# Kernel tuning notes

Measured on AMD Instinct MI355X. Metric: run time of the kernel, lower is better.

Reference implementation:

```python
import jax, jax.numpy as jnp
import numpy as np

ALPHA = 0.1
K = 10


def setup_inputs() -> dict:
    key = jax.random.key(0)
    ks = jax.random.split(key, 8)
    N, E, F_IN, H, C = 100000, 1600000, 256, 128, 16
    features = jax.random.normal(ks[0], (N, F_IN), dtype=jnp.float32)
    # Kaiming-ish small init so activations stay sane
    W0 = jax.random.normal(ks[1], (F_IN, H), dtype=jnp.float32) * (1.0 / np.sqrt(F_IN))
    b0 = jnp.zeros((H,), jnp.float32)
    W1 = jax.random.normal(ks[2], (H, H), dtype=jnp.float32) * (1.0 / np.sqrt(H))
    b1 = jnp.zeros((H,), jnp.float32)
    W2 = jax.random.normal(ks[3], (H, C), dtype=jnp.float32) * (1.0 / np.sqrt(H))
    b2 = jnp.zeros((C,), jnp.float32)
    src = jax.random.randint(ks[4], (E,), 0, N, dtype=jnp.int32)
    dst = jax.random.randint(ks[5], (E,), 0, N, dtype=jnp.int32)
    return {"features": features, "W0": W0, "b0": b0, "W1": W1, "b1": b1,
            "W2": W2, "b2": b2, "src": src, "dst": dst}


def reference(features, W0, b0, W1, b1, W2, b2, src, dst):
    N = features.shape[0]
    # --- MLP feature transform (feat_drop=0 -> identity) ---
    h = jax.nn.relu(features @ W0 + b0)
    h = jax.nn.relu(h @ W1 + b1)
    h = h @ W2 + b2  # [N, C]
    # --- symmetric normalization D_out^{-1/2} A D_in^{-1/2} (DGL APPNPConv) ---
    ones = jnp.ones(src.shape[0], dtype=h.dtype)
    out_deg = jax.ops.segment_sum(ones, src, num_segments=N)
    in_deg = jax.ops.segment_sum(ones, dst, num_segments=N)
    norm_src = jnp.where(out_deg > 0, jax.lax.rsqrt(jnp.maximum(out_deg, 1.0)), 0.0)[:, None]
    norm_dst = jnp.where(in_deg > 0, jax.lax.rsqrt(jnp.maximum(in_deg, 1.0)), 0.0)[:, None]
    # --- K-step personalized PageRank propagation (edge_drop=0) ---
    h0 = h
    for _ in range(K):
        msg = (h * norm_src)[src]                         # gather [E, C]
        agg = jax.ops.segment_sum(msg, dst, num_segments=N)  # scatter-add [N, C]
        h = (1.0 - ALPHA) * (agg * norm_dst) + ALPHA * h0
    return h
```

## Files before the change

### kernel.cpp

```cpp
#include <hip/hip_runtime.h>

typedef _Float16 half8 __attribute__((ext_vector_type(8)));
typedef _Float16 half4 __attribute__((ext_vector_type(4)));
typedef float f32x4 __attribute__((ext_vector_type(4)));
typedef unsigned short u16;
typedef unsigned int u32;

constexpr int F_IN = 256;
constexpr int H    = 128;
constexpr int C    = 16;
constexpr int KITER = 10;

constexpr int RANGE = 16384;
constexpr int PCH   = 128;


__global__ __launch_bounds__(256) void hist_k(const int* __restrict__ idx,
                                              u16* __restrict__ partial,
                                              int N, int E, int R, int chunk) {
    __shared__ unsigned int cnt[RANGE / 2];
    const int p  = blockIdx.x / R;
    const int r  = blockIdx.x % R;
    const int lo = r * RANGE;
    const int hi = min(lo + RANGE, N);
    const int t  = threadIdx.x;
    for (int i = t; i < RANGE / 2; i += 256) cnt[i] = 0;
    __syncthreads();
    const int e0 = p * chunk, e1 = min(e0 + chunk, E);
    for (int e = e0 + t; e < e1; e += 256) {
        int d = idx[e];
        if (d >= lo && d < hi) {
            int dl = d - lo;
            atomicAdd(&cnt[dl >> 1], 1u << ((dl & 1) << 4));
        }
    }
    __syncthreads();
    for (int i = lo + t; i < hi; i += 256) {
        int il = i - lo;
        partial[(size_t)p * N + i] = (u16)(cnt[il >> 1] >> ((il & 1) << 4));
    }
}

__global__ __launch_bounds__(256) void colsum_k(const u16* __restrict__ partial,
                                                int* __restrict__ deg, int N) {
    int i = blockIdx.x * 256 + threadIdx.x;
    if (i < N) {
        int s = 0;
#pragma unroll 8
        for (int p = 0; p < PCH; ++p) s += partial[(size_t)p * N + i];
        deg[i] = s;
    }
}

__global__ __launch_bounds__(256) void colprefix_norm_k(u16* __restrict__ partial,
                                                        const int* __restrict__ dego,
                                                        int* __restrict__ degi,
                                                        float* __restrict__ ns,
                                                        float* __restrict__ nd, int N) {
    int i = blockIdx.x * 256 + threadIdx.x;
    if (i < N) {
        int run = 0;
        for (int p = 0; p < PCH; ++p) {
            size_t q = (size_t)p * N + i;
            int v = partial[q];
            partial[q] = (u16)run;
            run += v;
        }
        degi[i] = run;
        int a = dego[i];
        ns[i] = (a > 0) ? rsqrtf((float)a) : 0.0f;
        nd[i] = (run > 0) ? rsqrtf((float)run) : 0.0f;
    }
}


__global__ __launch_bounds__(256) void scan1(const int* __restrict__ d, int* __restrict__ off,
                                             int* __restrict__ bsum, int N) {
    __shared__ int s[256];
    int t = threadIdx.x, i = blockIdx.x * 256 + t;
    int v = (i < N) ? d[i] : 0;
    s[t] = v;
    __syncthreads();
    for (int dd = 1; dd < 256; dd <<= 1) {
        int x = (t >= dd) ? s[t - dd] : 0;
        __syncthreads();
        s[t] += x;
        __syncthreads();
    }
    if (i < N) off[i] = s[t] - v;
    if (t == 255) bsum[blockIdx.x] = s[255];
}

__global__ __launch_bounds__(512) void scan2(int* __restrict__ bsum, int nb) {
    __shared__ int s[512];
    int t = threadIdx.x;
    int v = (t < nb) ? bsum[t] : 0;
    s[t] = v;
    __syncthreads();
    for (int dd = 1; dd < 512; dd <<= 1) {
        int x = (t >= dd) ? s[t - dd] : 0;
        __syncthreads();
        s[t] += x;
        __syncthreads();
    }
    if (t < nb) bsum[t] = s[t] - v;
}

__global__ __launch_bounds__(256) void scan3(int* __restrict__ off, const int* __restrict__ bsum,
                                             int N) {
    int i = blockIdx.x * 256 + threadIdx.x;
    if (i < N) off[i] += bsum[blockIdx.x];
}


__global__ __launch_bounds__(256) void scatter2_k(const int* __restrict__ src,
                                                  const int* __restrict__ dst,
                                                  const int* __restrict__ off,
                                                  const u16* __restrict__ pprefix,
                                                  u32* __restrict__ epack,
                                                  int N, int E, int R, int chunk) {
    __shared__ unsigned int cnt[RANGE / 2];
    const int p  = blockIdx.x / R;
    const int r  = blockIdx.x % R;
    const int lo = r * RANGE;
    const int hi = min(lo + RANGE, N);
    const int t  = threadIdx.x;
    for (int i = t; i < RANGE / 2; i += 256) cnt[i] = 0;
    __syncthreads();
    const int e0 = p * chunk, e1 = min(e0 + chunk, E);
    for (int e = e0 + t; e < e1; e += 256) {
        int d = dst[e];
        if (d >= lo && d < hi) {
            int dl    = d - lo;
            int shift = (dl & 1) << 4;
            unsigned int old = atomicAdd(&cnt[dl >> 1], 1u << shift);
            int rank = (int)((old >> shift) & 0xffffu);
            int pos = off[d] + (int)pprefix[(size_t)p * N + d] + rank;
            epack[pos] = (u32)src[e];
        }
    }
}


__global__ __launch_bounds__(256) void wpack(const float* __restrict__ W, half8* __restrict__ out,
                                             int K, int Ncols) {
    int tid = blockIdx.x * 256 + threadIdx.x;
    int KS = K / 32;
    int NT = Ncols / 16;
    int total = NT * KS * 64;
    if (tid < total) {
        int l  = tid & 63;
        int q  = tid >> 6;
        int nt = q % NT;
        int ks = q / NT;
        int col = nt * 16 + (l & 15);
        int kb  = ks * 32 + ((l >> 4) * 8);
        half8 h;
#pragma unroll
        for (int j = 0; j < 8; ++j) h[j] = (_Float16)W[(kb + j) * Ncols + col];
        out[tid] = h;
    }
}


__global__ __launch_bounds__(256, 4) void mlp_mfma(
    const float* __restrict__ feat,
    const half8* __restrict__ B0, const float* __restrict__ b0,
    const half8* __restrict__ B1, const float* __restrict__ b1,
    const half8* __restrict__ B2, const float* __restrict__ b2,
    const float* __restrict__ ns,
    float* __restrict__ h0out, _Float16* __restrict__ g0out, int N)
{
    __shared__ __align__(16) char lds[4 * 4096];
    const int t  = threadIdx.x;
    const int l  = t & 63;
    const int w  = t >> 6;
    const int cl = l & 15;
    const int qk = l >> 4;
    char* swp = lds + w * 4096;

    const int rowg = blockIdx.x * 64 + w * 16 + cl;
    const int rowc = (rowg < N) ? rowg : (N - 1);

    const float* ap = feat + (size_t)rowc * F_IN + qk * 8;
    half8 a0[8];
#pragma unroll
    for (int ks = 0; ks < 8; ++ks) {
        float4 f0 = *reinterpret_cast<const float4*>(ap + ks * 32);
        float4 f1 = *reinterpret_cast<const float4*>(ap + ks * 32 + 4);
        half8 h;
        h[0] = (_Float16)f0.x; h[1] = (_Float16)f0.y; h[2] = (_Float16)f0.z; h[3] = (_Float16)f0.w;
        h[4] = (_Float16)f1.x; h[5] = (_Float16)f1.y; h[6] = (_Float16)f1.z; h[7] = (_Float16)f1.w;
        a0[ks] = h;
    }
    f32x4 acc0[8];
#pragma unroll
    for (int nt = 0; nt < 8; ++nt) acc0[nt] = (f32x4){0.f, 0.f, 0.f, 0.f};
#pragma unroll
    for (int ks = 0; ks < 8; ++ks)
#pragma unroll
        for (int nt = 0; nt < 8; ++nt)
            acc0[nt] = __builtin_amdgcn_mfma_f32_16x16x32_f16(a0[ks], B0[(ks * 8 + nt) * 64 + l],
                                                              acc0[nt], 0, 0, 0);
#pragma unroll
    for (int nt = 0; nt < 8; ++nt) {
        float bb = b0[nt * 16 + cl];
#pragma unroll
        for (int r = 0; r < 4; ++r) {
            int orow = qk * 4 + r;
            int byte = orow * 256 + (((nt * 16 + cl) * 2) ^ ((orow & 7) << 4));
            *reinterpret_cast<_Float16*>(swp + byte) = (_Float16)fmaxf(acc0[nt][r] + bb, 0.0f);
        }
    }

    half8 a1[4];
#pragma unroll
    for (int ks = 0; ks < 4; ++ks) {
        int byte = cl * 256 + (((qk * 8 + ks * 32) * 2) ^ ((cl & 7) << 4));
        a1[ks] = *reinterpret_cast<const half8*>(swp + byte);
    }
    f32x4 acc1[8];
#pragma unroll
    for (int nt = 0; nt < 8; ++nt) acc1[nt] = (f32x4){0.f, 0.f, 0.f, 0.f};
#pragma unroll
    for (int ks = 0; ks < 4; ++ks)
#pragma unroll
        for (int nt = 0; nt < 8; ++nt)
            acc1[nt] = __builtin_amdgcn_mfma_f32_16x16x32_f16(a1[ks], B1[(ks * 8 + nt) * 64 + l],
                                                              acc1[nt], 0, 0, 0);
#pragma unroll
    for (int nt = 0; nt < 8; ++nt) {
        float bb = b1[nt * 16 + cl];
#pragma unroll
        for (int r = 0; r < 4; ++r) {
            int orow = qk * 4 + r;
            int byte = orow * 256 + (((nt * 16 + cl) * 2) ^ ((orow & 7) << 4));
            *reinterpret_cast<_Float16*>(swp + byte) = (_Float16)fmaxf(acc1[nt][r] + bb, 0.0f);
        }
    }

    f32x4 acc2 = (f32x4){0.f, 0.f, 0.f, 0.f};
#pragma unroll
    for (int ks = 0; ks < 4; ++ks) {
        int byte = cl * 256 + (((qk * 8 + ks * 32) * 2) ^ ((cl & 7) << 4));
        half8 a2 = *reinterpret_cast<const half8*>(swp + byte);
        acc2 = __builtin_amdgcn_mfma_f32_16x16x32_f16(a2, B2[ks * 64 + l], acc2, 0, 0, 0);
    }
    float bb2 = b2[cl];
#pragma unroll
    for (int r = 0; r < 4; ++r) {
        int orow = qk * 4 + r;
        int node = blockIdx.x * 64 + w * 16 + orow;
        if (node < N) {
            float hv = acc2[r] + bb2;
            h0out[(size_t)node * C + cl] = hv;
            g0out[(size_t)node * C + cl] = (_Float16)(hv * ns[node]);
        }
    }
}


__global__ __launch_bounds__(256) void gatherg(const u32* __restrict__ ep,
                                               const int* __restrict__ off,
                                               const half4* __restrict__ g,
                                               const float4* __restrict__ h0,
                                               const float* __restrict__ ns,
                                               const float* __restrict__ nd,
                                               half4* __restrict__ gnext,
                                               float4* __restrict__ hout,
                                               int N, int E, int last) {
    int gid = blockIdx.x * 256 + threadIdx.x;
    int node = gid >> 2;
    if (node >= N) return;
    int c = gid & 3;
    int o0 = off[node];
    int o1 = (node + 1 < N) ? off[node + 1] : E;
    float4 aA = {0.f, 0.f, 0.f, 0.f};
    float4 aB = {0.f, 0.f, 0.f, 0.f};
    float4 aC = {0.f, 0.f, 0.f, 0.f};
    float4 aD = {0.f, 0.f, 0.f, 0.f};
    int o = o0;
    for (; o + 4 <= o1; o += 4) {
        int s0 = (int)ep[o];
        int s1 = (int)ep[o + 1];
        int s2 = (int)ep[o + 2];
        int s3 = (int)ep[o + 3];
        half4 x0 = g[s0 * 4 + c];
        half4 x1 = g[s1 * 4 + c];
        half4 x2 = g[s2 * 4 + c];
        half4 x3 = g[s3 * 4 + c];
        aA.x += (float)x0[0]; aA.y += (float)x0[1]; aA.z += (float)x0[2]; aA.w += (float)x0[3];
        aB.x += (float)x1[0]; aB.y += (float)x1[1]; aB.z += (float)x1[2]; aB.w += (float)x1[3];
        aC.x += (float)x2[0]; aC.y += (float)x2[1]; aC.z += (float)x2[2]; aC.w += (float)x2[3];
        aD.x += (float)x3[0]; aD.y += (float)x3[1]; aD.z += (float)x3[2]; aD.w += (float)x3[3];
    }
    for (; o < o1; ++o) {
        int s0 = (int)ep[o];
        half4 x0 = g[s0 * 4 + c];
        aA.x += (float)x0[0]; aA.y += (float)x0[1]; aA.z += (float)x0[2]; aA.w += (float)x0[3];
    }
    aA.x += aB.x + aC.x + aD.x;
    aA.y += aB.y + aC.y + aD.y;
    aA.z += aB.z + aC.z + aD.z;
    aA.w += aB.w + aC.w + aD.w;
    float k = 0.9f * nd[node];
    float4 hv = h0[gid];
    float4 res;
    res.x = fmaf(k, aA.x, 0.1f * hv.x);
    res.y = fmaf(k, aA.y, 0.1f * hv.y);
    res.z = fmaf(k, aA.z, 0.1f * hv.z);
    res.w = fmaf(k, aA.w, 0.1f * hv.w);
    if (last) {
        hout[gid] = res;
    } else {
        float s = ns[node];
        half4 gv;
        gv[0] = (_Float16)(res.x * s);
        gv[1] = (_Float16)(res.y * s);
        gv[2] = (_Float16)(res.z * s);
        gv[3] = (_Float16)(res.w * s);
        gnext[gid] = gv;
    }
}


extern "C" void kernel_launch(void* const* d_in, const int* in_sizes, int n_in,
                              void* d_out, int out_size, void* d_ws, size_t ws_size,
                              hipStream_t stream) {
    const float* feat = (const float*)d_in[0];
    const float* W0   = (const float*)d_in[1];
    const float* b0   = (const float*)d_in[2];
    const float* W1   = (const float*)d_in[3];
    const float* b1   = (const float*)d_in[4];
    const float* W2   = (const float*)d_in[5];
    const float* b2   = (const float*)d_in[6];
    const int*   src  = (const int*)d_in[7];
    const int*   dst  = (const int*)d_in[8];

    const int N = in_sizes[0] / F_IN;
    const int E = in_sizes[7];
    const int NB = (N + 255) / 256;
    const int R  = (N + RANGE - 1) / RANGE;
    const int chunk = (E + PCH - 1) / PCH;

    char* base = (char*)d_ws;
    u16* part = (u16*)base;
    float*    h0 = (float*)base;
    _Float16* g0 = (_Float16*)(base + (size_t)N * C * 4);
    _Float16* ga = (_Float16*)(base + (size_t)N * C * 6);
    _Float16* gb = (_Float16*)(base + (size_t)N * C * 8);
    char* ws = base + (size_t)PCH * N * 2;
    int*   dego = (int*)ws;   ws += (size_t)N * 4;
    int*   degi = (int*)ws;   ws += (size_t)N * 4;
    float* ns   = (float*)ws; ws += (size_t)N * 4;
    float* nd   = (float*)ws; ws += (size_t)N * 4;
    int*   off  = (int*)ws;   ws += (size_t)N * 4;
    int*   bsum = (int*)ws;   ws += 512 * 4;
    u32*   epack = (u32*)ws;  ws += (size_t)E * 4;
    half8* B0 = (half8*)ws;   ws += 4096 * 16;
    half8* B1 = (half8*)ws;   ws += 2048 * 16;
    half8* B2 = (half8*)ws;   ws += 256 * 16;

    hist_k<<<PCH * R, 256, 0, stream>>>(src, part, N, E, R, chunk);
    colsum_k<<<NB, 256, 0, stream>>>(part, dego, N);
    hist_k<<<PCH * R, 256, 0, stream>>>(dst, part, N, E, R, chunk);
    colprefix_norm_k<<<NB, 256, 0, stream>>>(part, dego, degi, ns, nd, N);

    scan1<<<NB, 256, 0, stream>>>(degi, off, bsum, N);
    scan2<<<1, 512, 0, stream>>>(bsum, NB);
    scan3<<<NB, 256, 0, stream>>>(off, bsum, N);
    scatter2_k<<<PCH * R, 256, 0, stream>>>(src, dst, off, part, epack, N, E, R, chunk);

    wpack<<<16, 256, 0, stream>>>(W0, B0, 256, 128);
    wpack<<<8, 256, 0, stream>>>(W1, B1, 128, 128);
    wpack<<<1, 256, 0, stream>>>(W2, B2, 128, 16);
    mlp_mfma<<<(N + 63) / 64, 256, 0, stream>>>(feat, B0, b0, B1, b1, B2, b2, ns, h0, g0, N);

    const _Float16* curg = g0;
    for (int it = 0; it < KITER; ++it) {
        int last = (it == KITER - 1);
        _Float16* nxtg = (it & 1) ? gb : ga;
        gatherg<<<(N * 4 + 255) / 256, 256, 0, stream>>>(epack, off, (const half4*)curg,
                                                         (const float4*)h0, ns, nd,
                                                         (half4*)nxtg, (float4*)d_out, N, E, last);
        curg = nxtg;
    }
}
```

Measured before the change: 368.0 us.

## Record edge ranks in histogram, stage MLP weights in LDS, unroll gather

The dst histogram now stores each edge's intra-bin rank, so a flat one-thread-per-edge scatter pass replaces the second banded atomic scatter that rescanned every edge once per bin range. The three weight-pack launches are merged into one, and the MLP kernel moves to 768-thread blocks that copy all packed weights into about 148 KB of dynamic LDS instead of reading B fragments from global memory. The propagation gather unrolls its edge loop to 8 with a 2-wide tail and hoists its per-node loads ahead of the loop. The cost is an extra 2-byte-per-edge rank buffer and the occupancy limit imposed by the large LDS allocation.

```diff
diff --git a/kernel.cpp b/kernel.cpp
--- a/kernel.cpp
+++ b/kernel.cpp
@@ -32,6 +32,35 @@
         if (d >= lo && d < hi) {
             int dl = d - lo;
             atomicAdd(&cnt[dl >> 1], 1u << ((dl & 1) << 4));
+        }
+    }
+    __syncthreads();
+    for (int i = lo + t; i < hi; i += 256) {
+        int il = i - lo;
+        partial[(size_t)p * N + i] = (u16)(cnt[il >> 1] >> ((il & 1) << 4));
+    }
+}
+
+__global__ __launch_bounds__(256) void hist_rank_k(const int* __restrict__ idx,
+                                                   u16* __restrict__ partial,
+                                                   u16* __restrict__ rank16,
+                                                   int N, int E, int R, int chunk) {
+    __shared__ unsigned int cnt[RANGE / 2];
+    const int p  = blockIdx.x / R;
+    const int r  = blockIdx.x % R;
+    const int lo = r * RANGE;
+    const int hi = min(lo + RANGE, N);
+    const int t  = threadIdx.x;
+    for (int i = t; i < RANGE / 2; i += 256) cnt[i] = 0;
+    __syncthreads();
+    const int e0 = p * chunk, e1 = min(e0 + chunk, E);
+    for (int e = e0 + t; e < e1; e += 256) {
+        int d = idx[e];
+        if (d >= lo && d < hi) {
+            int dl    = d - lo;
+            int shift = (dl & 1) << 4;
+            unsigned int old = atomicAdd(&cnt[dl >> 1], 1u << shift);
+            rank16[e] = (u16)((old >> shift) & 0xffffu);
         }
     }
     __syncthreads();
@@ -113,86 +142,97 @@
 }
 
 
-__global__ __launch_bounds__(256) void scatter2_k(const int* __restrict__ src,
-                                                  const int* __restrict__ dst,
-                                                  const int* __restrict__ off,
-                                                  const u16* __restrict__ pprefix,
-                                                  u32* __restrict__ epack,
-                                                  int N, int E, int R, int chunk) {
-    __shared__ unsigned int cnt[RANGE / 2];
-    const int p  = blockIdx.x / R;
-    const int r  = blockIdx.x % R;
-    const int lo = r * RANGE;
-    const int hi = min(lo + RANGE, N);
-    const int t  = threadIdx.x;
-    for (int i = t; i < RANGE / 2; i += 256) cnt[i] = 0;
-    __syncthreads();
-    const int e0 = p * chunk, e1 = min(e0 + chunk, E);
-    for (int e = e0 + t; e < e1; e += 256) {
+__global__ __launch_bounds__(256) void scatter_pass(const int* __restrict__ src,
+                                                    const int* __restrict__ dst,
+                                                    const int* __restrict__ off,
+                                                    const u16* __restrict__ pprefix,
+                                                    const u16* __restrict__ rank16,
+                                                    u32* __restrict__ epack,
+                                                    int N, int E, int chunk) {
+    int e = blockIdx.x * 256 + threadIdx.x;
+    if (e < E) {
         int d = dst[e];
-        if (d >= lo && d < hi) {
-            int dl    = d - lo;
-            int shift = (dl & 1) << 4;
-            unsigned int old = atomicAdd(&cnt[dl >> 1], 1u << shift);
-            int rank = (int)((old >> shift) & 0xffffu);
-            int pos = off[d] + (int)pprefix[(size_t)p * N + d] + rank;
-            epack[pos] = (u32)src[e];
-        }
-    }
-}
-
-
-__global__ __launch_bounds__(256) void wpack(const float* __restrict__ W, half8* __restrict__ out,
-                                             int K, int Ncols) {
+        int p = e / chunk;
+        int pos = off[d] + (int)pprefix[(size_t)p * N + d] + (int)rank16[e];
+        epack[pos] = (u32)src[e];
+    }
+}
+
+
+__device__ inline void pack_one(const float* __restrict__ W, half8* __restrict__ out,
+                                int tid, int NT, int Ncols) {
+    int l  = tid & 63;
+    int q  = tid >> 6;
+    int nt = q % NT;
+    int ks = q / NT;
+    int col = nt * 16 + (l & 15);
+    int kb  = ks * 32 + ((l >> 4) * 8);
+    half8 h;
+#pragma unroll
+    for (int j = 0; j < 8; ++j) h[j] = (_Float16)W[(kb + j) * Ncols + col];
+    out[tid] = h;
+}
+
+__global__ __launch_bounds__(256) void wpack_all(const float* __restrict__ W0,
+                                                 const float* __restrict__ W1,
+                                                 const float* __restrict__ W2,
+                                                 half8* __restrict__ B0,
+                                                 half8* __restrict__ B1,
+                                                 half8* __restrict__ B2) {
     int tid = blockIdx.x * 256 + threadIdx.x;
-    int KS = K / 32;
-    int NT = Ncols / 16;
-    int total = NT * KS * 64;
-    if (tid < total) {
-        int l  = tid & 63;
-        int q  = tid >> 6;
-        int nt = q % NT;
-        int ks = q / NT;
-        int col = nt * 16 + (l & 15);
-        int kb  = ks * 32 + ((l >> 4) * 8);
-        half8 h;
-#pragma unroll
-        for (int j = 0; j < 8; ++j) h[j] = (_Float16)W[(kb + j) * Ncols + col];
-        out[tid] = h;
-    }
-}
-
-
-__global__ __launch_bounds__(256, 4) void mlp_mfma(
+    if (tid < 4096)      pack_one(W0, B0, tid, 8, 128);
+    else if (tid < 6144) pack_one(W1, B1, tid - 4096, 8, 128);
+    else if (tid < 6400) pack_one(W2, B2, tid - 6144, 1, 16);
+}
+
+
+__global__ __launch_bounds__(768, 3) void mlp_mega(
     const float* __restrict__ feat,
-    const half8* __restrict__ B0, const float* __restrict__ b0,
-    const half8* __restrict__ B1, const float* __restrict__ b1,
-    const half8* __restrict__ B2, const float* __restrict__ b2,
+    const float4* __restrict__ Bpack,
+    const float* __restrict__ b0, const float* __restrict__ b1, const float* __restrict__ b2,
     const float* __restrict__ ns,
     float* __restrict__ h0out, _Float16* __restrict__ g0out, int N)
 {
-    __shared__ __align__(16) char lds[4 * 4096];
+    extern __shared__ char lds[];
+    const half8* LB0 = (const half8*)lds;
+    const half8* LB1 = (const half8*)(lds + 65536);
+    const half8* LB2 = (const half8*)(lds + 98304);
+
     const int t  = threadIdx.x;
     const int l  = t & 63;
     const int w  = t >> 6;
     const int cl = l & 15;
     const int qk = l >> 4;
-    char* swp = lds + w * 4096;
-
-    const int rowg = blockIdx.x * 64 + w * 16 + cl;
+    char* swp = lds + 102400 + w * 4096;
+
+    const int rowg = blockIdx.x * 192 + w * 16 + cl;
     const int rowc = (rowg < N) ? rowg : (N - 1);
 
     const float* ap = feat + (size_t)rowc * F_IN + qk * 8;
+    float4 f[16];
+#pragma unroll
+    for (int ks = 0; ks < 8; ++ks) {
+        f[2 * ks]     = *reinterpret_cast<const float4*>(ap + ks * 32);
+        f[2 * ks + 1] = *reinterpret_cast<const float4*>(ap + ks * 32 + 4);
+    }
+
+    {
+        float4* ldst = (float4*)lds;
+        for (int i = t; i < 6400; i += 768) ldst[i] = Bpack[i];
+    }
+    __syncthreads();
+
     half8 a0[8];
 #pragma unroll
     for (int ks = 0; ks < 8; ++ks) {
-        float4 f0 = *reinterpret_cast<const float4*>(ap + ks * 32);
-        float4 f1 = *reinterpret_cast<const float4*>(ap + ks * 32 + 4);
         half8 h;
-        h[0] = (_Float16)f0.x; h[1] = (_Float16)f0.y; h[2] = (_Float16)f0.z; h[3] = (_Float16)f0.w;
-        h[4] = (_Float16)f1.x; h[5] = (_Float16)f1.y; h[6] = (_Float16)f1.z; h[7] = (_Float16)f1.w;
+        h[0] = (_Float16)f[2 * ks].x; h[1] = (_Float16)f[2 * ks].y;
+        h[2] = (_Float16)f[2 * ks].z; h[3] = (_Float16)f[2 * ks].w;
+        h[4] = (_Float16)f[2 * ks + 1].x; h[5] = (_Float16)f[2 * ks + 1].y;
+        h[6] = (_Float16)f[2 * ks + 1].z; h[7] = (_Float16)f[2 * ks + 1].w;
         a0[ks] = h;
     }
+
     f32x4 acc0[8];
 #pragma unroll
     for (int nt = 0; nt < 8; ++nt) acc0[nt] = (f32x4){0.f, 0.f, 0.f, 0.f};
@@ -200,7 +240,7 @@
     for (int ks = 0; ks < 8; ++ks)
 #pragma unroll
         for (int nt = 0; nt < 8; ++nt)
-            acc0[nt] = __builtin_amdgcn_mfma_f32_16x16x32_f16(a0[ks], B0[(ks * 8 + nt) * 64 + l],
+            acc0[nt] = __builtin_amdgcn_mfma_f32_16x16x32_f16(a0[ks], LB0[(ks * 8 + nt) * 64 + l],
                                                               acc0[nt], 0, 0, 0);
 #pragma unroll
     for (int nt = 0; nt < 8; ++nt) {
@@ -226,7 +266,7 @@
     for (int ks = 0; ks < 4; ++ks)
 #pragma unroll
         for (int nt = 0; nt < 8; ++nt)
-            acc1[nt] = __builtin_amdgcn_mfma_f32_16x16x32_f16(a1[ks], B1[(ks * 8 + nt) * 64 + l],
+            acc1[nt] = __builtin_amdgcn_mfma_f32_16x16x32_f16(a1[ks], LB1[(ks * 8 + nt) * 64 + l],
                                                               acc1[nt], 0, 0, 0);
 #pragma unroll
     for (int nt = 0; nt < 8; ++nt) {
@@ -244,13 +284,13 @@
     for (int ks = 0; ks < 4; ++ks) {
         int byte = cl * 256 + (((qk * 8 + ks * 32) * 2) ^ ((cl & 7) << 4));
         half8 a2 = *reinterpret_cast<const half8*>(swp + byte);
-        acc2 = __builtin_amdgcn_mfma_f32_16x16x32_f16(a2, B2[ks * 64 + l], acc2, 0, 0, 0);
+        acc2 = __builtin_amdgcn_mfma_f32_16x16x32_f16(a2, LB2[ks * 64 + l], acc2, 0, 0, 0);
     }
     float bb2 = b2[cl];
 #pragma unroll
     for (int r = 0; r < 4; ++r) {
         int orow = qk * 4 + r;
-        int node = blockIdx.x * 64 + w * 16 + orow;
+        int node = blockIdx.x * 192 + w * 16 + orow;
         if (node < N) {
             float hv = acc2[r] + bb2;
             h0out[(size_t)node * C + cl] = hv;
@@ -275,26 +315,41 @@
     int c = gid & 3;
     int o0 = off[node];
     int o1 = (node + 1 < N) ? off[node + 1] : E;
+    float k  = 0.9f * nd[node];
+    float sc = ns[node];
+    float4 hv = h0[gid];
     float4 aA = {0.f, 0.f, 0.f, 0.f};
     float4 aB = {0.f, 0.f, 0.f, 0.f};
     float4 aC = {0.f, 0.f, 0.f, 0.f};
     float4 aD = {0.f, 0.f, 0.f, 0.f};
     int o = o0;
-    for (; o + 4 <= o1; o += 4) {
-        int s0 = (int)ep[o];
-        int s1 = (int)ep[o + 1];
-        int s2 = (int)ep[o + 2];
-        int s3 = (int)ep[o + 3];
-        half4 x0 = g[s0 * 4 + c];
-        half4 x1 = g[s1 * 4 + c];
-        half4 x2 = g[s2 * 4 + c];
-        half4 x3 = g[s3 * 4 + c];
+    for (; o + 8 <= o1; o += 8) {
+        int s0 = (int)ep[o];     int s1 = (int)ep[o + 1];
+        int s2 = (int)ep[o + 2]; int s3 = (int)ep[o + 3];
+        int s4 = (int)ep[o + 4]; int s5 = (int)ep[o + 5];
+        int s6 = (int)ep[o + 6]; int s7 = (int)ep[o + 7];
+        half4 x0 = g[s0 * 4 + c]; half4 x1 = g[s1 * 4 + c];
+        half4 x2 = g[s2 * 4 + c]; half4 x3 = g[s3 * 4 + c];
+        half4 x4 = g[s4 * 4 + c]; half4 x5 = g[s5 * 4 + c];
+        half4 x6 = g[s6 * 4 + c]; half4 x7 = g[s7 * 4 + c];
         aA.x += (float)x0[0]; aA.y += (float)x0[1]; aA.z += (float)x0[2]; aA.w += (float)x0[3];
         aB.x += (float)x1[0]; aB.y += (float)x1[1]; aB.z += (float)x1[2]; aB.w += (float)x1[3];
         aC.x += (float)x2[0]; aC.y += (float)x2[1]; aC.z += (float)x2[2]; aC.w += (float)x2[3];
         aD.x += (float)x3[0]; aD.y += (float)x3[1]; aD.z += (float)x3[2]; aD.w += (float)x3[3];
-    }
-    for (; o < o1; ++o) {
+        aA.x += (float)x4[0]; aA.y += (float)x4[1]; aA.z += (float)x4[2]; aA.w += (float)x4[3];
+        aB.x += (float)x5[0]; aB.y += (float)x5[1]; aB.z += (float)x5[2]; aB.w += (float)x5[3];
+        aC.x += (float)x6[0]; aC.y += (float)x6[1]; aC.z += (float)x6[2]; aC.w += (float)x6[3];
+        aD.x += (float)x7[0]; aD.y += (float)x7[1]; aD.z += (float)x7[2]; aD.w += (float)x7[3];
+    }
+    for (; o + 2 <= o1; o += 2) {
+        int s0 = (int)ep[o];
+        int s1 = (int)ep[o + 1];
+        half4 x0 = g[s0 * 4 + c];
+        half4 x1 = g[s1 * 4 + c];
+        aA.x += (float)x0[0]; aA.y += (float)x0[1]; aA.z += (float)x0[2]; aA.w += (float)x0[3];
+        aB.x += (float)x1[0]; aB.y += (float)x1[1]; aB.z += (float)x1[2]; aB.w += (float)x1[3];
+    }
+    if (o < o1) {
         int s0 = (int)ep[o];
         half4 x0 = g[s0 * 4 + c];
         aA.x += (float)x0[0]; aA.y += (float)x0[1]; aA.z += (float)x0[2]; aA.w += (float)x0[3];
@@ -303,8 +358,6 @@
     aA.y += aB.y + aC.y + aD.y;
     aA.z += aB.z + aC.z + aD.z;
     aA.w += aB.w + aC.w + aD.w;
-    float k = 0.9f * nd[node];
-    float4 hv = h0[gid];
     float4 res;
     res.x = fmaf(k, aA.x, 0.1f * hv.x);
     res.y = fmaf(k, aA.y, 0.1f * hv.y);
@@ -313,12 +366,11 @@
     if (last) {
         hout[gid] = res;
     } else {
-        float s = ns[node];
         half4 gv;
-        gv[0] = (_Float16)(res.x * s);
-        gv[1] = (_Float16)(res.y * s);
-        gv[2] = (_Float16)(res.z * s);
-        gv[3] = (_Float16)(res.w * s);
+        gv[0] = (_Float16)(res.x * sc);
+        gv[1] = (_Float16)(res.y * sc);
+        gv[2] = (_Float16)(res.z * sc);
+        gv[3] = (_Float16)(res.w * sc);
         gnext[gid] = gv;
     }
 }
@@ -356,25 +408,25 @@
     float* nd   = (float*)ws; ws += (size_t)N * 4;
     int*   off  = (int*)ws;   ws += (size_t)N * 4;
     int*   bsum = (int*)ws;   ws += 512 * 4;
-    u32*   epack = (u32*)ws;  ws += (size_t)E * 4;
+    u16*   rank16 = (u16*)ws; ws += (size_t)E * 2;
+    u32*   epack  = (u32*)ws; ws += (size_t)E * 4;
     half8* B0 = (half8*)ws;   ws += 4096 * 16;
     half8* B1 = (half8*)ws;   ws += 2048 * 16;
     half8* B2 = (half8*)ws;   ws += 256 * 16;
 
     hist_k<<<PCH * R, 256, 0, stream>>>(src, part, N, E, R, chunk);
     colsum_k<<<NB, 256, 0, stream>>>(part, dego, N);
-    hist_k<<<PCH * R, 256, 0, stream>>>(dst, part, N, E, R, chunk);
+    hist_rank_k<<<PCH * R, 256, 0, stream>>>(dst, part, rank16, N, E, R, chunk);
     colprefix_norm_k<<<NB, 256, 0, stream>>>(part, dego, degi, ns, nd, N);
 
     scan1<<<NB, 256, 0, stream>>>(degi, off, bsum, N);
     scan2<<<1, 512, 0, stream>>>(bsum, NB);
     scan3<<<NB, 256, 0, stream>>>(off, bsum, N);
-    scatter2_k<<<PCH * R, 256, 0, stream>>>(src, dst, off, part, epack, N, E, R, chunk);
-
-    wpack<<<16, 256, 0, stream>>>(W0, B0, 256, 128);
-    wpack<<<8, 256, 0, stream>>>(W1, B1, 128, 128);
-    wpack<<<1, 256, 0, stream>>>(W2, B2, 128, 16);
-    mlp_mfma<<<(N + 63) / 64, 256, 0, stream>>>(feat, B0, b0, B1, b1, B2, b2, ns, h0, g0, N);
+    scatter_pass<<<(E + 255) / 256, 256, 0, stream>>>(src, dst, off, part, rank16, epack, N, E, chunk);
+
+    wpack_all<<<25, 256, 0, stream>>>(W0, W1, W2, B0, B1, B2);
+    mlp_mega<<<(N + 191) / 192, 768, 151552, stream>>>(feat, (const float4*)B0, b0, b1, b2,
+                                                       ns, h0, g0, N);
 
     const _Float16* curg = g0;
     for (int it = 0; it < KITER; ++it) {
```

After: 345.2 us. 1.07x faster.
